# Performance work log

Measured on AMD Instinct MI355X. Metric: run time of the kernel, lower is better.

## Reference

```python
import jax, jax.numpy as jnp
import numpy as np

NUM_HEADS = 16
D_MODEL = 1024
DEPTH = D_MODEL // NUM_HEADS
B, S = 4, 1024  # q,k seq len = S; v seq len = S-1


def setup_inputs() -> dict:
    key = jax.random.key(0)
    ks = jax.random.split(key, 6)
    scale = 1.0 / np.sqrt(D_MODEL)
    return {
        "v": jax.random.normal(ks[0], (B, S - 1, D_MODEL), dtype=jnp.float32),
        "k": jax.random.normal(ks[1], (B, S, D_MODEL), dtype=jnp.float32),
        "q": jax.random.normal(ks[2], (B, S, D_MODEL), dtype=jnp.float32),
        "mask": jnp.zeros((B, S - 1, S - 1), dtype=jnp.float32),
        "Wv": jax.random.normal(ks[3], (D_MODEL, D_MODEL), dtype=jnp.float32) * scale,
        "bv": jnp.zeros((D_MODEL,), dtype=jnp.float32),
        "Wd": jax.random.normal(ks[4], (D_MODEL, D_MODEL), dtype=jnp.float32) * scale,
        "bd": jnp.zeros((D_MODEL,), dtype=jnp.float32),
    }


def _split_heads(x):
    # (B, T, d_model) -> (B, H, T, depth)
    b, t, _ = x.shape
    return x.reshape(b, t, NUM_HEADS, DEPTH).transpose(0, 2, 1, 3)


def reference(v, k, q, mask, Wv, bv, Wd, bd):
    # 3-D q/k path: qq=q, kk=k (q_layers/k_layers/wq/wk unused)
    vv = v @ Wv + bv                       # (B, S-1, d_model)
    qh = _split_heads(q)                   # (B, H, S, depth)
    kh = _split_heads(k)                   # (B, H, S, depth)
    vh = _split_heads(vv)                  # (B, H, S-1, depth)

    scores = jnp.einsum('bhqd,bhkd->bhqk', qh, kh)      # (B, H, S, S)
    scores = scores[:, :, 1:, :-1]                      # (B, H, S-1, S-1)
    dk = jnp.asarray(DEPTH, scores.dtype)
    nl = jax.nn.relu(scores / jnp.sqrt(dk))
    nl = nl + mask[:, None, :, :] * (-1e9)
    att = jax.nn.softmax(nl, axis=-1)                   # (B, H, S-1, S-1)

    out = jnp.einsum('bhqk,bhkd->bhqd', att, vh)        # (B, H, S-1, depth)
    out = out.transpose(0, 2, 1, 3).reshape(v.shape[0], -1, D_MODEL)  # (B, S-1, d_model)
    output = out @ Wd + bd
    return output, att
```

## Files before the change

kernel.cpp:

```cpp
#include <hip/hip_runtime.h>
#include <hip/hip_bf16.h>

#define NUM_HEADS 16
#define DM 1024
#define DEPTH 64
#define BB 4
#define SS 1024
#define SL 1023
#define M_ROWS (BB*SL)

typedef __attribute__((ext_vector_type(8))) short short8;
typedef __attribute__((ext_vector_type(4))) float floatx4;

__device__ inline unsigned short f2bf(float f) {
  __hip_bfloat16 hb = __float2bfloat16(f);
  return *reinterpret_cast<unsigned short*>(&hb);
}
__device__ inline short8 ld_frag(const unsigned short* p) {
  return *reinterpret_cast<const short8*>(p);
}

#define SWZ(row, g) (((g) ^ ((row) & 7)))

#define GLDS(g, l) __builtin_amdgcn_global_load_lds( \
    (const __attribute__((address_space(1))) void*)(g), \
    (__attribute__((address_space(3))) void*)(l), 16, 0, 0)

__global__ __launch_bounds__(256) void f32_to_bf16_vec(
    const float* __restrict__ in, unsigned short* __restrict__ out, int n8)
{
  int i = blockIdx.x * 256 + threadIdx.x;
  if (i >= n8) return;
  const float4 f0 = ((const float4*)in)[(size_t)i * 2];
  const float4 f1 = ((const float4*)in)[(size_t)i * 2 + 1];
  unsigned short t[8];
  t[0]=f2bf(f0.x); t[1]=f2bf(f0.y); t[2]=f2bf(f0.z); t[3]=f2bf(f0.w);
  t[4]=f2bf(f1.x); t[5]=f2bf(f1.y); t[6]=f2bf(f1.z); t[7]=f2bf(f1.w);
  ((uint4*)out)[i] = *(uint4*)t;
}

__global__ __launch_bounds__(256) void transpose_to_bf16(
    const float* __restrict__ W, unsigned short* __restrict__ WT)
{
  __shared__ unsigned short tile[64][72];
  const int tid = threadIdx.x;
  const int k0 = blockIdx.y * 64, n0 = blockIdx.x * 64;
  {
    const int kl = tid >> 2, nc = (tid & 3) * 16;
    const float* src = W + (size_t)(k0 + kl) * DM + n0 + nc;
    #pragma unroll
    for (int j = 0; j < 16; j += 4) {
      float4 f = *(const float4*)(src + j);
      tile[nc + j + 0][kl] = f2bf(f.x);
      tile[nc + j + 1][kl] = f2bf(f.y);
      tile[nc + j + 2][kl] = f2bf(f.z);
      tile[nc + j + 3][kl] = f2bf(f.w);
    }
  }
  __syncthreads();
  {
    const int nl = tid >> 2, kc = (tid & 3) * 16;
    unsigned short tmp[16];
    #pragma unroll
    for (int j = 0; j < 16; j++) tmp[j] = tile[nl][kc + j];
    unsigned short* dst = WT + (size_t)(n0 + nl) * DM + k0 + kc;
    *(uint4*)&dst[0] = *(uint4*)&tmp[0];
    *(uint4*)&dst[8] = *(uint4*)&tmp[8];
  }
}

template <bool OUT_BF16>
__global__ __launch_bounds__(256) void gemm_bt(
    const unsigned short* __restrict__ A,
    const unsigned short* __restrict__ BT,
    const float* __restrict__ bias,
    void* __restrict__ Cv, int M)
{
  constexpr int BM = 64, BN = 128, BK = 64;
  __shared__ __align__(16) unsigned short As[3][BM * BK];
  __shared__ __align__(16) unsigned short Bs[3][BN * BK];

  const int tid = threadIdx.x;
  const int w = tid >> 6, lane = tid & 63, q4 = lane >> 4, l16 = lane & 15;
  const int wm = w >> 1, wn = w & 1;
  const int rb = blockIdx.y * BM;
  const int cb = blockIdx.x * BN;

  const int wbase = __builtin_amdgcn_readfirstlane(w * 512);

  const int srow = tid >> 3;
  const int lg   = (tid & 7) ^ (srow & 7);
  int ar0 = rb + srow;       if (ar0 >= M) ar0 = M - 1;
  int ar1 = rb + 32 + srow;  if (ar1 >= M) ar1 = M - 1;
  const unsigned short* a_src0 = A + (size_t)ar0 * DM + lg * 8;
  const unsigned short* a_src1 = A + (size_t)ar1 * DM + lg * 8;
  const unsigned short* b_src0 = BT + (size_t)(cb      + srow) * DM + lg * 8;
  const unsigned short* b_src1 = BT + (size_t)(cb + 32 + srow) * DM + lg * 8;
  const unsigned short* b_src2 = BT + (size_t)(cb + 64 + srow) * DM + lg * 8;
  const unsigned short* b_src3 = BT + (size_t)(cb + 96 + srow) * DM + lg * 8;

  auto stage = [&](int t, unsigned short* Ab, unsigned short* Bb) {
    const int kn = t * BK;
    GLDS(a_src0 + kn, Ab + wbase);
    GLDS(a_src1 + kn, Ab + 2048 + wbase);
    GLDS(b_src0 + kn, Bb + wbase);
    GLDS(b_src1 + kn, Bb + 2048 + wbase);
    GLDS(b_src2 + kn, Bb + 4096 + wbase);
    GLDS(b_src3 + kn, Bb + 6144 + wbase);
  };

  int aoff[2][2], boff[4][2];
  #pragma unroll
  for (int i = 0; i < 2; i++)
    #pragma unroll
    for (int hf = 0; hf < 2; hf++) {
      int r = wm * 32 + i * 16 + l16;
      aoff[i][hf] = r * BK + SWZ(r, q4 + 4 * hf) * 8;
    }
  #pragma unroll
  for (int j = 0; j < 4; j++)
    #pragma unroll
    for (int hf = 0; hf < 2; hf++) {
      int r = wn * 64 + j * 16 + l16;
      boff[j][hf] = r * BK + SWZ(r, q4 + 4 * hf) * 8;
    }

  floatx4 acc[2][4];
  #pragma unroll
  for (int i = 0; i < 2; i++)
    #pragma unroll
    for (int j = 0; j < 4; j++) acc[i][j] = (floatx4){0.f,0.f,0.f,0.f};

  stage(0, As[0], Bs[0]);
  stage(1, As[1], Bs[1]);
  stage(2, As[2], Bs[2]);

  int cur = 0;
  constexpr int NT = DM / BK;
  for (int t = 0; t < NT; ++t) {
    if (t < NT - 2)       asm volatile("s_waitcnt vmcnt(12)" ::: "memory");
    else if (t == NT - 2) asm volatile("s_waitcnt vmcnt(6)"  ::: "memory");
    else                  asm volatile("s_waitcnt vmcnt(0)"  ::: "memory");
    __builtin_amdgcn_sched_barrier(0);
    __builtin_amdgcn_s_barrier();
    __builtin_amdgcn_sched_barrier(0);

    unsigned short* Ab = As[cur];
    unsigned short* Bb = Bs[cur];
    short8 af[2][2], bfr[4][2];
    #pragma unroll
    for (int hf = 0; hf < 2; hf++) {
      af[0][hf] = ld_frag(Ab + aoff[0][hf]);
      af[1][hf] = ld_frag(Ab + aoff[1][hf]);
      bfr[0][hf] = ld_frag(Bb + boff[0][hf]);
      bfr[1][hf] = ld_frag(Bb + boff[1][hf]);
      bfr[2][hf] = ld_frag(Bb + boff[2][hf]);
      bfr[3][hf] = ld_frag(Bb + boff[3][hf]);
    }
    asm volatile("s_waitcnt lgkmcnt(0)" ::: "memory");
    __builtin_amdgcn_sched_barrier(0);
    __builtin_amdgcn_s_barrier();
    __builtin_amdgcn_sched_barrier(0);

    if (t + 3 < NT) stage(t + 3, Ab, Bb);

    #pragma unroll
    for (int hf = 0; hf < 2; hf++) {
      acc[0][0] = __builtin_amdgcn_mfma_f32_16x16x32_bf16(af[0][hf], bfr[0][hf], acc[0][0], 0,0,0);
      acc[0][1] = __builtin_amdgcn_mfma_f32_16x16x32_bf16(af[0][hf], bfr[1][hf], acc[0][1], 0,0,0);
      acc[0][2] = __builtin_amdgcn_mfma_f32_16x16x32_bf16(af[0][hf], bfr[2][hf], acc[0][2], 0,0,0);
      acc[0][3] = __builtin_amdgcn_mfma_f32_16x16x32_bf16(af[0][hf], bfr[3][hf], acc[0][3], 0,0,0);
      acc[1][0] = __builtin_amdgcn_mfma_f32_16x16x32_bf16(af[1][hf], bfr[0][hf], acc[1][0], 0,0,0);
      acc[1][1] = __builtin_amdgcn_mfma_f32_16x16x32_bf16(af[1][hf], bfr[1][hf], acc[1][1], 0,0,0);
      acc[1][2] = __builtin_amdgcn_mfma_f32_16x16x32_bf16(af[1][hf], bfr[2][hf], acc[1][2], 0,0,0);
      acc[1][3] = __builtin_amdgcn_mfma_f32_16x16x32_bf16(af[1][hf], bfr[3][hf], acc[1][3], 0,0,0);
    }
    cur = (cur == 2) ? 0 : cur + 1;
  }

  #pragma unroll
  for (int j = 0; j < 4; j++) {
    int col = cb + wn * 64 + j * 16 + l16;
    float bb = bias[col];
    #pragma unroll
    for (int i = 0; i < 2; i++) {
      #pragma unroll
      for (int r = 0; r < 4; r++) {
        int m = rb + wm * 32 + i * 16 + q4 * 4 + r;
        if (m < M) {
          float val = acc[i][j][r] + bb;
          if (OUT_BF16) ((unsigned short*)Cv)[(size_t)m * DM + col] = f2bf(val);
          else __builtin_nontemporal_store(val, &((float*)Cv)[(size_t)m * DM + col]);
        }
      }
    }
  }
}

__global__ __launch_bounds__(256) void attn_kernel(
    const float* __restrict__ Q, const float* __restrict__ Kg,
    const float* __restrict__ Mask, const unsigned short* __restrict__ VV,
    float* __restrict__ Att, unsigned short* __restrict__ Out2)
{
  const int h = blockIdx.x, qt = blockIdx.y, b = blockIdx.z;
  const int tid = threadIdx.x;
  const int w = tid >> 6, lane = tid & 63, q4 = lane >> 4, l16 = lane & 15;
  const int qi0 = qt * 64;
  const int qb = w * 16;

  __shared__ unsigned short qsh[64][72];
  __shared__ unsigned short ksh[64][72];
  __shared__ unsigned short vshT[64][72];
  __shared__ unsigned short psh[4][16][72];

  {
    int qr = tid >> 2, d0 = (tid & 3) * 16;
    int qi = qi0 + qr;
    unsigned short tmp[16];
    if (qi < SL) {
      const float* src = Q + ((size_t)b * SS + qi + 1) * DM + h * DEPTH + d0;
      #pragma unroll
      for (int j = 0; j < 16; j += 4) {
        float4 f = *(const float4*)(src + j);
        tmp[j+0]=f2bf(f.x); tmp[j+1]=f2bf(f.y); tmp[j+2]=f2bf(f.z); tmp[j+3]=f2bf(f.w);
      }
    } else {
      #pragma unroll
      for (int j = 0; j < 16; j++) tmp[j] = 0;
    }
    *(uint4*)&qsh[qr][d0]     = *(uint4*)&tmp[0];
    *(uint4*)&qsh[qr][d0 + 8] = *(uint4*)&tmp[8];
  }

  auto stageK = [&](int kt) {
    int kr = tid >> 2, d0 = (tid & 3) * 16;
    int kj = kt * 64 + kr;
    unsigned short tmp[16];
    if (kj < SL) {
      const float* src = Kg + ((size_t)b * SS + kj) * DM + h * DEPTH + d0;
      #pragma unroll
      for (int j = 0; j < 16; j += 4) {
        float4 f = *(const float4*)(src + j);
        tmp[j+0]=f2bf(f.x); tmp[j+1]=f2bf(f.y); tmp[j+2]=f2bf(f.z); tmp[j+3]=f2bf(f.w);
      }
    } else {
      #pragma unroll
      for (int j = 0; j < 16; j++) tmp[j] = 0;
    }
    *(uint4*)&ksh[kr][d0]     = *(uint4*)&tmp[0];
    *(uint4*)&ksh[kr][d0 + 8] = *(uint4*)&tmp[8];
  };

  auto stageV = [&](int kt) {
    int d = tid & 63, k16 = (tid >> 6) * 16;
    unsigned short tmp[16];
    #pragma unroll
    for (int j = 0; j < 16; j++) {
      int kj = kt * 64 + k16 + j;
      tmp[j] = (kj < SL) ? VV[((size_t)b * SL + kj) * DM + h * DEPTH + d] : (unsigned short)0;
    }
    *(uint4*)&vshT[d][k16]     = *(uint4*)&tmp[0];
    *(uint4*)&vshT[d][k16 + 8] = *(uint4*)&tmp[8];
  };

  __syncthreads();

  float rsv[4] = {0.f, 0.f, 0.f, 0.f};
  for (int kt = 0; kt < 16; kt++) {
    __syncthreads();
    stageK(kt);
    __syncthreads();
    #pragma unroll
    for (int nt = 0; nt < 4; nt++) {
      floatx4 s = (floatx4){0.f,0.f,0.f,0.f};
      s = __builtin_amdgcn_mfma_f32_16x16x32_bf16(
            ld_frag(&qsh[qb + l16][q4*8]), ld_frag(&ksh[nt*16 + l16][q4*8]), s, 0,0,0);
      s = __builtin_amdgcn_mfma_f32_16x16x32_bf16(
            ld_frag(&qsh[qb + l16][32 + q4*8]), ld_frag(&ksh[nt*16 + l16][32 + q4*8]), s, 0,0,0);
      int kj = kt * 64 + nt * 16 + l16;
      bool kv = kj < SL;
      int qi_b = qi0 + qb + q4 * 4;
      const float* mp = Mask + ((size_t)b * SL + qi_b) * SL + kj;
      #pragma unroll
      for (int r = 0; r < 4; r++) {
        int qi = qi_b + r;
        float mval = (kv && qi < SL) ? mp[(size_t)r * SL] : 0.f;
        float sv = fmaxf(s[r] * 0.125f, 0.f) + mval * (-1e9f);
        float p = kv ? __expf(sv) : 0.f;
        rsv[r] += p;
      }
    }
  }
  #pragma unroll
  for (int r = 0; r < 4; r++) {
    #pragma unroll
    for (int off = 1; off < 16; off <<= 1) rsv[r] += __shfl_xor(rsv[r], off, 64);
  }
  float inv[4];
  #pragma unroll
  for (int r = 0; r < 4; r++) inv[r] = 1.f / rsv[r];

  floatx4 oacc[4];
  #pragma unroll
  for (int i = 0; i < 4; i++) oacc[i] = (floatx4){0.f,0.f,0.f,0.f};

  for (int kt = 0; kt < 16; kt++) {
    __syncthreads();
    stageK(kt);
    stageV(kt);
    __syncthreads();
    #pragma unroll
    for (int nt = 0; nt < 4; nt++) {
      floatx4 s = (floatx4){0.f,0.f,0.f,0.f};
      s = __builtin_amdgcn_mfma_f32_16x16x32_bf16(
            ld_frag(&qsh[qb + l16][q4*8]), ld_frag(&ksh[nt*16 + l16][q4*8]), s, 0,0,0);
      s = __builtin_amdgcn_mfma_f32_16x16x32_bf16(
            ld_frag(&qsh[qb + l16][32 + q4*8]), ld_frag(&ksh[nt*16 + l16][32 + q4*8]), s, 0,0,0);
      int kj = kt * 64 + nt * 16 + l16;
      bool kv = kj < SL;
      int qi_b = qi0 + qb + q4 * 4;
      const float* mp = Mask + ((size_t)b * SL + qi_b) * SL + kj;
      #pragma unroll
      for (int r = 0; r < 4; r++) {
        int qi = qi_b + r;
        bool qv = qi < SL;
        float mval = (kv && qv) ? mp[(size_t)r * SL] : 0.f;
        float sv = fmaxf(s[r] * 0.125f, 0.f) + mval * (-1e9f);
        float p = kv ? __expf(sv) : 0.f;
        float pn = p * inv[r];
        if (kv && qv)
          Att[(((size_t)(b * NUM_HEADS + h)) * SL + qi) * SL + kj] = pn;
        psh[w][q4 * 4 + r][nt * 16 + l16] = f2bf(pn);
      }
    }
    short8 pa0 = ld_frag(&psh[w][l16][q4 * 8]);
    short8 pa1 = ld_frag(&psh[w][l16][32 + q4 * 8]);
    #pragma unroll
    for (int nt2 = 0; nt2 < 4; nt2++) {
      oacc[nt2] = __builtin_amdgcn_mfma_f32_16x16x32_bf16(
                    pa0, ld_frag(&vshT[nt2*16 + l16][q4*8]), oacc[nt2], 0,0,0);
      oacc[nt2] = __builtin_amdgcn_mfma_f32_16x16x32_bf16(
                    pa1, ld_frag(&vshT[nt2*16 + l16][32 + q4*8]), oacc[nt2], 0,0,0);
    }
  }

  #pragma unroll
  for (int nt2 = 0; nt2 < 4; nt2++) {
    #pragma unroll
    for (int r = 0; r < 4; r++) {
      int qi = qi0 + qb + q4 * 4 + r;
      if (qi < SL)
        Out2[((size_t)b * SL + qi) * DM + h * DEPTH + nt2 * 16 + l16] = f2bf(oacc[nt2][r]);
    }
  }
}

extern "C" void kernel_launch(void* const* d_in, const int* in_sizes, int n_in,
                              void* d_out, int out_size, void* d_ws, size_t ws_size,
                              hipStream_t stream) {
  const float* v    = (const float*)d_in[0];
  const float* k    = (const float*)d_in[1];
  const float* q    = (const float*)d_in[2];
  const float* mask = (const float*)d_in[3];
  const float* Wv   = (const float*)d_in[4];
  const float* bv   = (const float*)d_in[5];
  const float* Wd   = (const float*)d_in[6];
  const float* bd   = (const float*)d_in[7];

  float* out = (float*)d_out;
  float* att = out + (size_t)M_ROWS * DM;
  unsigned short* vv   = (unsigned short*)d_ws;
  unsigned short* out2 = vv + (size_t)M_ROWS * DM;

  unsigned short* WvT = (unsigned short*)att;
  unsigned short* vbf = WvT + (size_t)DM * DM;
  unsigned short* WdT = vv;

  const int n8 = (M_ROWS * DM) / 8;

  f32_to_bf16_vec<<<dim3((n8 + 255) / 256), 256, 0, stream>>>(v, vbf, n8);
  transpose_to_bf16<<<dim3(16, 16), 256, 0, stream>>>(Wv, WvT);
  gemm_bt<true><<<dim3(DM/128, (M_ROWS+63)/64), 256, 0, stream>>>(vbf, WvT, bv, (void*)vv, M_ROWS);
  attn_kernel<<<dim3(NUM_HEADS, 16, BB), 256, 0, stream>>>(q, k, mask, vv, att, out2);
  transpose_to_bf16<<<dim3(16, 16), 256, 0, stream>>>(Wd, WdT);
  gemm_bt<false><<<dim3(DM/128, (M_ROWS+63)/64), 256, 0, stream>>>(out2, WdT, bd, (void*)out, M_ROWS);
}
```

Baseline: 643.5 us.

## Pre-convert Q/K to bf16 and pre-transpose V for attention

After: 656.4 us. 1.02x slower.

```diff
diff --git a/kernel.cpp b/kernel.cpp
--- a/kernel.cpp
+++ b/kernel.cpp
@@ -39,6 +39,24 @@
   ((uint4*)out)[i] = *(uint4*)t;
 }
 
+__global__ __launch_bounds__(256) void conv_rows_bf16(
+    const float* __restrict__ in, unsigned short* __restrict__ out, int rowoff)
+{
+  int i = blockIdx.x * 256 + threadIdx.x;
+  const int n8 = (M_ROWS * DM) / 8;
+  if (i >= n8) return;
+  int row = i >> 7;
+  int g = i & 127;
+  int b = row / SL, r = row - b * SL;
+  const float* src = in + ((size_t)b * SS + r + rowoff) * DM + g * 8;
+  const float4 f0 = ((const float4*)src)[0];
+  const float4 f1 = ((const float4*)src)[1];
+  unsigned short t[8];
+  t[0]=f2bf(f0.x); t[1]=f2bf(f0.y); t[2]=f2bf(f0.z); t[3]=f2bf(f0.w);
+  t[4]=f2bf(f1.x); t[5]=f2bf(f1.y); t[6]=f2bf(f1.z); t[7]=f2bf(f1.w);
+  *(uint4*)(out + (size_t)row * DM + g * 8) = *(uint4*)t;
+}
+
 __global__ __launch_bounds__(256) void transpose_to_bf16(
     const float* __restrict__ W, unsigned short* __restrict__ WT)
 {
@@ -64,6 +82,39 @@
     #pragma unroll
     for (int j = 0; j < 16; j++) tmp[j] = tile[nl][kc + j];
     unsigned short* dst = WT + (size_t)(n0 + nl) * DM + k0 + kc;
+    *(uint4*)&dst[0] = *(uint4*)&tmp[0];
+    *(uint4*)&dst[8] = *(uint4*)&tmp[8];
+  }
+}
+
+__global__ __launch_bounds__(256) void transpose_v(
+    const unsigned short* __restrict__ VV, unsigned short* __restrict__ VvT)
+{
+  __shared__ unsigned short tile[64][72];
+  const int kt = blockIdx.x, h = blockIdx.y, b = blockIdx.z;
+  const int tid = threadIdx.x;
+  {
+    const int kr = tid >> 2, c = (tid & 3) * 16;
+    const int kj = kt * 64 + kr;
+    unsigned short tmp[16];
+    if (kj < SL) {
+      const unsigned short* s = VV + ((size_t)b * SL + kj) * DM + h * DEPTH + c;
+      *(uint4*)&tmp[0] = *(const uint4*)s;
+      *(uint4*)&tmp[8] = *(const uint4*)(s + 8);
+    } else {
+      #pragma unroll
+      for (int j = 0; j < 16; j++) tmp[j] = 0;
+    }
+    #pragma unroll
+    for (int j = 0; j < 16; j++) tile[c + j][kr] = tmp[j];
+  }
+  __syncthreads();
+  {
+    const int d = tid >> 2, k16 = (tid & 3) * 16;
+    unsigned short tmp[16];
+    #pragma unroll
+    for (int j = 0; j < 16; j++) tmp[j] = tile[d][k16 + j];
+    unsigned short* dst = VvT + (((size_t)(b * NUM_HEADS + h)) * DEPTH + d) * 1024 + kt * 64 + k16;
     *(uint4*)&dst[0] = *(uint4*)&tmp[0];
     *(uint4*)&dst[8] = *(uint4*)&tmp[8];
   }
@@ -83,8 +134,11 @@
   const int tid = threadIdx.x;
   const int w = tid >> 6, lane = tid & 63, q4 = lane >> 4, l16 = lane & 15;
   const int wm = w >> 1, wn = w & 1;
-  const int rb = blockIdx.y * BM;
-  const int cb = blockIdx.x * BN;
+
+  const int flat = blockIdx.y * gridDim.x + blockIdx.x;
+  const int nf = (flat & 7) * ((int)(gridDim.x * gridDim.y) >> 3) + (flat >> 3);
+  const int rb = (nf >> 3) * BM;
+  const int cb = (nf & 7) * BN;
 
   const int wbase = __builtin_amdgcn_readfirstlane(w * 512);
 
@@ -197,9 +251,10 @@
   }
 }
 
-__global__ __launch_bounds__(256) void attn_kernel(
-    const float* __restrict__ Q, const float* __restrict__ Kg,
-    const float* __restrict__ Mask, const unsigned short* __restrict__ VV,
+__global__ __launch_bounds__(256) void attn_bf(
+    const unsigned short* __restrict__ Qbf,
+    const unsigned short* __restrict__ Kbf,
+    const float* __restrict__ Mask, const unsigned short* __restrict__ VvT,
     float* __restrict__ Att, unsigned short* __restrict__ Out2)
 {
   const int h = blockIdx.x, qt = blockIdx.y, b = blockIdx.z;
@@ -214,56 +269,44 @@
   __shared__ unsigned short psh[4][16][72];
 
   {
-    int qr = tid >> 2, d0 = (tid & 3) * 16;
-    int qi = qi0 + qr;
-    unsigned short tmp[16];
+    const int qr = tid >> 2, d0 = (tid & 3) * 16;
+    const int qi = qi0 + qr;
     if (qi < SL) {
-      const float* src = Q + ((size_t)b * SS + qi + 1) * DM + h * DEPTH + d0;
-      #pragma unroll
-      for (int j = 0; j < 16; j += 4) {
-        float4 f = *(const float4*)(src + j);
-        tmp[j+0]=f2bf(f.x); tmp[j+1]=f2bf(f.y); tmp[j+2]=f2bf(f.z); tmp[j+3]=f2bf(f.w);
-      }
+      const unsigned short* s = Qbf + ((size_t)b * SL + qi) * DM + h * DEPTH + d0;
+      *(uint4*)&qsh[qr][d0]     = *(const uint4*)s;
+      *(uint4*)&qsh[qr][d0 + 8] = *(const uint4*)(s + 8);
     } else {
-      #pragma unroll
-      for (int j = 0; j < 16; j++) tmp[j] = 0;
-    }
-    *(uint4*)&qsh[qr][d0]     = *(uint4*)&tmp[0];
-    *(uint4*)&qsh[qr][d0 + 8] = *(uint4*)&tmp[8];
+      uint4 z = {0,0,0,0};
+      *(uint4*)&qsh[qr][d0] = z;
+      *(uint4*)&qsh[qr][d0 + 8] = z;
+    }
   }
 
   auto stageK = [&](int kt) {
-    int kr = tid >> 2, d0 = (tid & 3) * 16;
-    int kj = kt * 64 + kr;
-    unsigned short tmp[16];
+    const int kr = tid >> 2, d0 = (tid & 3) * 16;
+    const int kj = kt * 64 + kr;
     if (kj < SL) {
-      const float* src = Kg + ((size_t)b * SS + kj) * DM + h * DEPTH + d0;
-      #pragma unroll
-      for (int j = 0; j < 16; j += 4) {
-        float4 f = *(const float4*)(src + j);
-        tmp[j+0]=f2bf(f.x); tmp[j+1]=f2bf(f.y); tmp[j+2]=f2bf(f.z); tmp[j+3]=f2bf(f.w);
-      }
+      const unsigned short* s = Kbf + ((size_t)b * SL + kj) * DM + h * DEPTH + d0;
+      *(uint4*)&ksh[kr][d0]     = *(const uint4*)s;
+      *(uint4*)&ksh[kr][d0 + 8] = *(const uint4*)(s + 8);
     } else {
-      #pragma unroll
-      for (int j = 0; j < 16; j++) tmp[j] = 0;
-    }
-    *(uint4*)&ksh[kr][d0]     = *(uint4*)&tmp[0];
-    *(uint4*)&ksh[kr][d0 + 8] = *(uint4*)&tmp[8];
+      uint4 z = {0,0,0,0};
+      *(uint4*)&ksh[kr][d0] = z;
+      *(uint4*)&ksh[kr][d0 + 8] = z;
+    }
   };
-
   auto stageV = [&](int kt) {
-    int d = tid & 63, k16 = (tid >> 6) * 16;
-    unsigned short tmp[16];
-    #pragma unroll
-    for (int j = 0; j < 16; j++) {
-      int kj = kt * 64 + k16 + j;
-      tmp[j] = (kj < SL) ? VV[((size_t)b * SL + kj) * DM + h * DEPTH + d] : (unsigned short)0;
-    }
-    *(uint4*)&vshT[d][k16]     = *(uint4*)&tmp[0];
-    *(uint4*)&vshT[d][k16 + 8] = *(uint4*)&tmp[8];
+    const int d = tid >> 2, c = (tid & 3) * 16;
+    const unsigned short* s = VvT + (((size_t)(b * NUM_HEADS + h)) * DEPTH + d) * 1024 + kt * 64 + c;
+    *(uint4*)&vshT[d][c]     = *(const uint4*)s;
+    *(uint4*)&vshT[d][c + 8] = *(const uint4*)(s + 8);
   };
 
   __syncthreads();
+
+  const short8 qf0 = ld_frag(&qsh[qb + l16][q4 * 8]);
+  const short8 qf1 = ld_frag(&qsh[qb + l16][32 + q4 * 8]);
+  const int qi_b = qi0 + qb + q4 * 4;
 
   float rsv[4] = {0.f, 0.f, 0.f, 0.f};
   for (int kt = 0; kt < 16; kt++) {
@@ -274,12 +317,11 @@
     for (int nt = 0; nt < 4; nt++) {
       floatx4 s = (floatx4){0.f,0.f,0.f,0.f};
       s = __builtin_amdgcn_mfma_f32_16x16x32_bf16(
-            ld_frag(&qsh[qb + l16][q4*8]), ld_frag(&ksh[nt*16 + l16][q4*8]), s, 0,0,0);
-      s = __builtin_amdgcn_mfma_f32_16x16x32_bf16(
-            ld_frag(&qsh[qb + l16][32 + q4*8]), ld_frag(&ksh[nt*16 + l16][32 + q4*8]), s, 0,0,0);
+            qf0, ld_frag(&ksh[nt*16 + l16][q4*8]), s, 0,0,0);
+      s = __builtin_amdgcn_mfma_f32_16x16x32_bf16(
+            qf1, ld_frag(&ksh[nt*16 + l16][32 + q4*8]), s, 0,0,0);
       int kj = kt * 64 + nt * 16 + l16;
       bool kv = kj < SL;
-      int qi_b = qi0 + qb + q4 * 4;
       const float* mp = Mask + ((size_t)b * SL + qi_b) * SL + kj;
       #pragma unroll
       for (int r = 0; r < 4; r++) {
@@ -313,12 +355,11 @@
     for (int nt = 0; nt < 4; nt++) {
       floatx4 s = (floatx4){0.f,0.f,0.f,0.f};
       s = __builtin_amdgcn_mfma_f32_16x16x32_bf16(
-            ld_frag(&qsh[qb + l16][q4*8]), ld_frag(&ksh[nt*16 + l16][q4*8]), s, 0,0,0);
-      s = __builtin_amdgcn_mfma_f32_16x16x32_bf16(
-            ld_frag(&qsh[qb + l16][32 + q4*8]), ld_frag(&ksh[nt*16 + l16][32 + q4*8]), s, 0,0,0);
+            qf0, ld_frag(&ksh[nt*16 + l16][q4*8]), s, 0,0,0);
+      s = __builtin_amdgcn_mfma_f32_16x16x32_bf16(
+            qf1, ld_frag(&ksh[nt*16 + l16][32 + q4*8]), s, 0,0,0);
       int kj = kt * 64 + nt * 16 + l16;
       bool kv = kj < SL;
-      int qi_b = qi0 + qb + q4 * 4;
       const float* mp = Mask + ((size_t)b * SL + qi_b) * SL + kj;
       #pragma unroll
       for (int r = 0; r < 4; r++) {
@@ -355,6 +396,164 @@
   }
 }
 
+__global__ __launch_bounds__(256) void attn_f32(
+    const float* __restrict__ Q, const float* __restrict__ Kg,
+    const float* __restrict__ Mask, const unsigned short* __restrict__ VV,
+    float* __restrict__ Att, unsigned short* __restrict__ Out2)
+{
+  const int h = blockIdx.x, qt = blockIdx.y, b = blockIdx.z;
+  const int tid = threadIdx.x;
+  const int w = tid >> 6, lane = tid & 63, q4 = lane >> 4, l16 = lane & 15;
+  const int qi0 = qt * 64;
+  const int qb = w * 16;
+
+  __shared__ unsigned short qsh[64][72];
+  __shared__ unsigned short ksh[64][72];
+  __shared__ unsigned short vshT[64][72];
+  __shared__ unsigned short psh[4][16][72];
+
+  {
+    int qr = tid >> 2, d0 = (tid & 3) * 16;
+    int qi = qi0 + qr;
+    unsigned short tmp[16];
+    if (qi < SL) {
+      const float* src = Q + ((size_t)b * SS + qi + 1) * DM + h * DEPTH + d0;
+      #pragma unroll
+      for (int j = 0; j < 16; j += 4) {
+        float4 f = *(const float4*)(src + j);
+        tmp[j+0]=f2bf(f.x); tmp[j+1]=f2bf(f.y); tmp[j+2]=f2bf(f.z); tmp[j+3]=f2bf(f.w);
+      }
+    } else {
+      #pragma unroll
+      for (int j = 0; j < 16; j++) tmp[j] = 0;
+    }
+    *(uint4*)&qsh[qr][d0]     = *(uint4*)&tmp[0];
+    *(uint4*)&qsh[qr][d0 + 8] = *(uint4*)&tmp[8];
+  }
+
+  auto stageK = [&](int kt) {
+    int kr = tid >> 2, d0 = (tid & 3) * 16;
+    int kj = kt * 64 + kr;
+    unsigned short tmp[16];
+    if (kj < SL) {
+      const float* src = Kg + ((size_t)b * SS + kj) * DM + h * DEPTH + d0;
+      #pragma unroll
+      for (int j = 0; j < 16; j += 4) {
+        float4 f = *(const float4*)(src + j);
+        tmp[j+0]=f2bf(f.x); tmp[j+1]=f2bf(f.y); tmp[j+2]=f2bf(f.z); tmp[j+3]=f2bf(f.w);
+      }
+    } else {
+      #pragma unroll
+      for (int j = 0; j < 16; j++) tmp[j] = 0;
+    }
+    *(uint4*)&ksh[kr][d0]     = *(uint4*)&tmp[0];
+    *(uint4*)&ksh[kr][d0 + 8] = *(uint4*)&tmp[8];
+  };
+
+  auto stageV = [&](int kt) {
+    int d = tid & 63, k16 = (tid >> 6) * 16;
+    unsigned short tmp[16];
+    #pragma unroll
+    for (int j = 0; j < 16; j++) {
+      int kj = kt * 64 + k16 + j;
+      tmp[j] = (kj < SL) ? VV[((size_t)b * SL + kj) * DM + h * DEPTH + d] : (unsigned short)0;
+    }
+    *(uint4*)&vshT[d][k16]     = *(uint4*)&tmp[0];
+    *(uint4*)&vshT[d][k16 + 8] = *(uint4*)&tmp[8];
+  };
+
+  __syncthreads();
+
+  float rsv[4] = {0.f, 0.f, 0.f, 0.f};
+  for (int kt = 0; kt < 16; kt++) {
+    __syncthreads();
+    stageK(kt);
+    __syncthreads();
+    #pragma unroll
+    for (int nt = 0; nt < 4; nt++) {
+      floatx4 s = (floatx4){0.f,0.f,0.f,0.f};
+      s = __builtin_amdgcn_mfma_f32_16x16x32_bf16(
+            ld_frag(&qsh[qb + l16][q4*8]), ld_frag(&ksh[nt*16 + l16][q4*8]), s, 0,0,0);
+      s = __builtin_amdgcn_mfma_f32_16x16x32_bf16(
+            ld_frag(&qsh[qb + l16][32 + q4*8]), ld_frag(&ksh[nt*16 + l16][32 + q4*8]), s, 0,0,0);
+      int kj = kt * 64 + nt * 16 + l16;
+      bool kv = kj < SL;
+      int qi_b = qi0 + qb + q4 * 4;
+      const float* mp = Mask + ((size_t)b * SL + qi_b) * SL + kj;
+      #pragma unroll
+      for (int r = 0; r < 4; r++) {
+        int qi = qi_b + r;
+        float mval = (kv && qi < SL) ? mp[(size_t)r * SL] : 0.f;
+        float sv = fmaxf(s[r] * 0.125f, 0.f) + mval * (-1e9f);
+        float p = kv ? __expf(sv) : 0.f;
+        rsv[r] += p;
+      }
+    }
+  }
+  #pragma unroll
+  for (int r = 0; r < 4; r++) {
+    #pragma unroll
+    for (int off = 1; off < 16; off <<= 1) rsv[r] += __shfl_xor(rsv[r], off, 64);
+  }
+  float inv[4];
+  #pragma unroll
+  for (int r = 0; r < 4; r++) inv[r] = 1.f / rsv[r];
+
+  floatx4 oacc[4];
+  #pragma unroll
+  for (int i = 0; i < 4; i++) oacc[i] = (floatx4){0.f,0.f,0.f,0.f};
+
+  for (int kt = 0; kt < 16; kt++) {
+    __syncthreads();
+    stageK(kt);
+    stageV(kt);
+    __syncthreads();
+    #pragma unroll
+    for (int nt = 0; nt < 4; nt++) {
+      floatx4 s = (floatx4){0.f,0.f,0.f,0.f};
+      s = __builtin_amdgcn_mfma_f32_16x16x32_bf16(
+            ld_frag(&qsh[qb + l16][q4*8]), ld_frag(&ksh[nt*16 + l16][q4*8]), s, 0,0,0);
+      s = __builtin_amdgcn_mfma_f32_16x16x32_bf16(
+            ld_frag(&qsh[qb + l16][32 + q4*8]), ld_frag(&ksh[nt*16 + l16][32 + q4*8]), s, 0,0,0);
+      int kj = kt * 64 + nt * 16 + l16;
+      bool kv = kj < SL;
+      int qi_b = qi0 + qb + q4 * 4;
+      const float* mp = Mask + ((size_t)b * SL + qi_b) * SL + kj;
+      #pragma unroll
+      for (int r = 0; r < 4; r++) {
+        int qi = qi_b + r;
+        bool qv = qi < SL;
+        float mval = (kv && qv) ? mp[(size_t)r * SL] : 0.f;
+        float sv = fmaxf(s[r] * 0.125f, 0.f) + mval * (-1e9f);
+        float p = kv ? __expf(sv) : 0.f;
+        float pn = p * inv[r];
+        if (kv && qv)
+          Att[(((size_t)(b * NUM_HEADS + h)) * SL + qi) * SL + kj] = pn;
+        psh[w][q4 * 4 + r][nt * 16 + l16] = f2bf(pn);
+      }
+    }
+    short8 pa0 = ld_frag(&psh[w][l16][q4 * 8]);
+    short8 pa1 = ld_frag(&psh[w][l16][32 + q4 * 8]);
+    #pragma unroll
+    for (int nt2 = 0; nt2 < 4; nt2++) {
+      oacc[nt2] = __builtin_amdgcn_mfma_f32_16x16x32_bf16(
+                    pa0, ld_frag(&vshT[nt2*16 + l16][q4*8]), oacc[nt2], 0,0,0);
+      oacc[nt2] = __builtin_amdgcn_mfma_f32_16x16x32_bf16(
+                    pa1, ld_frag(&vshT[nt2*16 + l16][32 + q4*8]), oacc[nt2], 0,0,0);
+    }
+  }
+
+  #pragma unroll
+  for (int nt2 = 0; nt2 < 4; nt2++) {
+    #pragma unroll
+    for (int r = 0; r < 4; r++) {
+      int qi = qi0 + qb + q4 * 4 + r;
+      if (qi < SL)
+        Out2[((size_t)b * SL + qi) * DM + h * DEPTH + nt2 * 16 + l16] = f2bf(oacc[nt2][r]);
+    }
+  }
+}
+
 extern "C" void kernel_launch(void* const* d_in, const int* in_sizes, int n_in,
                               void* d_out, int out_size, void* d_ws, size_t ws_size,
                               hipStream_t stream) {
@@ -376,12 +575,39 @@
   unsigned short* vbf = WvT + (size_t)DM * DM;
   unsigned short* WdT = vv;
 
-  const int n8 = (M_ROWS * DM) / 8;
-
-  f32_to_bf16_vec<<<dim3((n8 + 255) / 256), 256, 0, stream>>>(v, vbf, n8);
+  const size_t N = (size_t)M_ROWS * DM;
+  const size_t NV = (size_t)BB * NUM_HEADS * DEPTH * 1024;
+  const size_t need_full = 2 * (2 * N + 2 * N + NV) / 2;
+  const size_t full_bytes = (2 * N + 2 * N + NV) * 2;
+  const size_t mid_bytes  = (2 * N + NV) * 2;
+  (void)need_full;
+
+  const int n8v = (int)(N / 8);
+
+  f32_to_bf16_vec<<<dim3((n8v + 255) / 256), 256, 0, stream>>>(v, vbf, n8v);
   transpose_to_bf16<<<dim3(16, 16), 256, 0, stream>>>(Wv, WvT);
   gemm_bt<true><<<dim3(DM/128, (M_ROWS+63)/64), 256, 0, stream>>>(vbf, WvT, bv, (void*)vv, M_ROWS);
-  attn_kernel<<<dim3(NUM_HEADS, 16, BB), 256, 0, stream>>>(q, k, mask, vv, att, out2);
+
+  if (ws_size >= full_bytes) {
+    unsigned short* qbf = out2 + N;
+    unsigned short* kbf = qbf + N;
+    unsigned short* VvT = kbf + N;
+    conv_rows_bf16<<<dim3((n8v + 255) / 256), 256, 0, stream>>>(q, qbf, 1);
+    conv_rows_bf16<<<dim3((n8v + 255) / 256), 256, 0, stream>>>(k, kbf, 0);
+    transpose_v<<<dim3(16, NUM_HEADS, BB), 256, 0, stream>>>(vv, VvT);
+    attn_bf<<<dim3(NUM_HEADS, 16, BB), 256, 0, stream>>>(qbf, kbf, mask, VvT, att, out2);
+  } else if (ws_size >= mid_bytes) {
+    unsigned short* qbf = (unsigned short*)out;
+    unsigned short* kbf = qbf + N;
+    unsigned short* VvT = out2 + N;
+    conv_rows_bf16<<<dim3((n8v + 255) / 256), 256, 0, stream>>>(q, qbf, 1);
+    conv_rows_bf16<<<dim3((n8v + 255) / 256), 256, 0, stream>>>(k, kbf, 0);
+    transpose_v<<<dim3(16, NUM_HEADS, BB), 256, 0, stream>>>(vv, VvT);
+    attn_bf<<<dim3(NUM_HEADS, 16, BB), 256, 0, stream>>>(qbf, kbf, mask, VvT, att, out2);
+  } else {
+    attn_f32<<<dim3(NUM_HEADS, 16, BB), 256, 0, stream>>>(q, k, mask, vv, att, out2);
+  }
+
   transpose_to_bf16<<<dim3(16, 16), 256, 0, stream>>>(Wd, WdT);
   gemm_bt<false><<<dim3(DM/128, (M_ROWS+63)/64), 256, 0, stream>>>(out2, WdT, bd, (void*)out, M_ROWS);
 }
```
